# Kernel tuning notes

Measured on AMD Instinct MI355X. Metric: run time of the kernel, lower is better.

Reference implementation:

```python
import math
import jax, jax.numpy as jnp
import numpy as np

S, D_IN, H = 512, 256, 512  # seq_len(=num_events, window=1), input_dim, hidden_dim


def _ln(x, g, b, eps=1e-5):
    m = x.mean(-1, keepdims=True)
    v = ((x - m) ** 2).mean(-1, keepdims=True)
    return (x - m) * jax.lax.rsqrt(v + eps) * g + b


def setup_inputs() -> dict:
    key = jax.random.key(0)
    ks = jax.random.split(key, 16)
    p = lambda k, shp: (0.02 * jax.random.normal(k, shp, dtype=jnp.float32))
    return {
        "timestamps": jax.random.uniform(ks[0], (S,), dtype=jnp.float32),
        "features": jax.random.normal(ks[1], (S, D_IN), dtype=jnp.float32),
        "amplitudes": jax.random.uniform(ks[2], (S,), dtype=jnp.float32),
        "neuron_ids": jax.random.randint(ks[3], (S,), 0, 4096, dtype=jnp.int64 if jax.config.jax_enable_x64 else jnp.int32),
        # event_encoder: Linear(D_IN, H//2) -> ReLU -> Linear(H//2, H) -> LayerNorm(H)
        "We1": p(ks[4], (D_IN, H // 2)), "be1": jnp.zeros((H // 2,), jnp.float32),
        "We2": p(ks[5], (H // 2, H)), "be2": jnp.zeros((H,), jnp.float32),
        "g_ev": jnp.ones((H,), jnp.float32), "b_ev": jnp.zeros((H,), jnp.float32),
        # temporal_encoder: Linear(1, H//4) -> ReLU -> Linear(H//4, H//2)
        "Wt1": p(ks[6], (1, H // 4)), "bt1": jnp.zeros((H // 4,), jnp.float32),
        "Wt2": p(ks[7], (H // 4, H // 2)), "bt2": jnp.zeros((H // 2,), jnp.float32),
        # connectivity_proj: Linear(2H, H)  (used to map concat -> H)
        "Wc": p(ks[8], (2 * H, H)), "bc": jnp.zeros((H,), jnp.float32),
        # spike_rate_norm: LayerNorm(H)
        "g_sr": jnp.ones((H,), jnp.float32), "b_sr": jnp.zeros((H,), jnp.float32),
        # q/k/v projections Linear(H, H)
        "Wq": p(ks[9], (H, H)), "bq": jnp.zeros((H,), jnp.float32),
        "Wk": p(ks[10], (H, H)), "bk": jnp.zeros((H,), jnp.float32),
        "Wv": p(ks[11], (H, H)), "bv": jnp.zeros((H,), jnp.float32),
    }


def reference(timestamps, features, amplitudes, neuron_ids,
              We1, be1, We2, be2, g_ev, b_ev,
              Wt1, bt1, Wt2, bt2, Wc, bc, g_sr, b_sr,
              Wq, bq, Wk, bk, Wv, bv):
    s = features.shape[0]
    h_dim = Wq.shape[0]
    # _group_events_by_window with window_size=1: sort by timestamp
    order = jnp.argsort(timestamps)
    ts = timestamps[order]
    feats = features[order]
    amps = amplitudes[order]
    # event encoding: MLP + LayerNorm -> [S, H]
    h = jnp.maximum(feats @ We1 + be1, 0.0) @ We2 + be2
    h = _ln(h, g_ev, b_ev)
    # temporal encoding of raw timestamps -> [S, H/2], tiled to [S, H]
    t = jnp.maximum(ts[:, None] @ Wt1 + bt1, 0.0) @ Wt2 + bt2
    rep = h.shape[-1] // t.shape[-1]  # = 2
    comb = jnp.concatenate([h, jnp.tile(t, (1, rep))], axis=-1)  # [S, 2H]
    comb = comb * amps[:, None]                                   # amplitude gating
    comb = comb @ Wc + bc                                         # project 2H -> H
    comb = _ln(comb, g_sr, b_sr)
    # sinusoidal positional (temporal) encoding [S, H]
    pos = jnp.arange(s, dtype=jnp.float32)[:, None]
    div = jnp.exp(jnp.arange(0, h_dim, 2, dtype=jnp.float32) * (-math.log(10000.0) / h_dim))
    ang = pos * div  # [S, H/2]
    te = jnp.stack([jnp.sin(ang), jnp.cos(ang)], axis=-1).reshape(s, h_dim)
    ctx = (comb + te)[None]  # [1, S, H]
    # connectivity bias: 1 / (1 + |i - j|)  (vectorized; diagonal = 1 matches eye)
    idx = jnp.arange(s)
    conn = 1.0 / (1.0 + jnp.abs(idx[:, None] - idx[None, :]).astype(jnp.float32))  # [S, S]
    Q = ctx @ Wq + bq                                   # [1, S, H]
    K = ctx @ Wk + bk + conn[:, :, None] * 0.1          # broadcast -> [S, S, H]
    V = ctx @ Wv + bv                                   # [1, S, H]
    return Q, K, V
```

## Files before the change

### kernel.cpp

```cpp
#include <hip/hip_runtime.h>
#include <math.h>

#define S 512
#define DIN 256
#define H 512

typedef float f4 __attribute__((ext_vector_type(4)));

__global__ __launch_bounds__(512) void sort_kernel(
    const float* __restrict__ ts, const float* __restrict__ amp,
    int* __restrict__ order, float* __restrict__ ts_s, float* __restrict__ amp_s)
{
    __shared__ float sts[S];
    int i = threadIdx.x;
    sts[i] = ts[i];
    __syncthreads();
    float ti = sts[i];
    int rank = 0;
    for (int j = 0; j < S; ++j) {
        float tj = sts[j];
        rank += (tj < ti) || (tj == ti && j < i);
    }
    order[rank] = i;
    ts_s[rank]  = ti;
    amp_s[rank] = amp[i];
}

__device__ __forceinline__ void block_stats_512(float s, float ss, float* red,
                                                float& mean, float& inv)
{
    for (int off = 32; off > 0; off >>= 1) {
        s  += __shfl_down(s, off);
        ss += __shfl_down(ss, off);
    }
    int wid = threadIdx.x >> 6;
    if ((threadIdx.x & 63) == 0) { red[wid] = s; red[4 + wid] = ss; }
    __syncthreads();
    if (threadIdx.x == 0) {
        float Sm  = red[0] + red[1] + red[2] + red[3];
        float SSm = red[4] + red[5] + red[6] + red[7];
        float m = Sm * (1.0f / 512.0f);
        float v = SSm * (1.0f / 512.0f) - m * m;
        red[8] = m;
        red[9] = rsqrtf(v + 1e-5f);
    }
    __syncthreads();
    mean = red[8];
    inv  = red[9];
}

__global__ __launch_bounds__(256) void encoder_kernel(
    const int* __restrict__ order, const float* __restrict__ ts_s,
    const float* __restrict__ amp_s, const float* __restrict__ feats,
    const float* __restrict__ We1, const float* __restrict__ be1,
    const float* __restrict__ We2, const float* __restrict__ be2,
    const float* __restrict__ g_ev, const float* __restrict__ b_ev,
    const float* __restrict__ Wt1, const float* __restrict__ bt1,
    const float* __restrict__ Wt2, const float* __restrict__ bt2,
    const float* __restrict__ Wc, const float* __restrict__ bc,
    const float* __restrict__ g_sr, const float* __restrict__ b_sr,
    float* __restrict__ ctx)
{
    __shared__ float sf[DIN];
    __shared__ float sh1[256];
    __shared__ float sth[128];
    __shared__ float scomb[1024];
    __shared__ float red[16];

    int r = blockIdx.x;
    int t = threadIdx.x;
    int o = order[r];
    sf[t] = feats[o * DIN + t];
    float x = ts_s[r];
    if (t < 128) sth[t] = fmaxf(fmaf(x, Wt1[t], bt1[t]), 0.0f);
    __syncthreads();

    float acc = be1[t];
    #pragma unroll 4
    for (int d = 0; d < DIN; ++d) acc = fmaf(sf[d], We1[d * 256 + t], acc);
    sh1[t] = fmaxf(acc, 0.0f);
    __syncthreads();

    float a0 = be2[t], a1 = be2[t + 256];
    #pragma unroll 4
    for (int k = 0; k < 256; ++k) {
        float hv = sh1[k];
        a0 = fmaf(hv, We2[k * 512 + t], a0);
        a1 = fmaf(hv, We2[k * 512 + t + 256], a1);
    }
    float m, inv;
    block_stats_512(a0 + a1, a0 * a0 + a1 * a1, red, m, inv);
    float ampv = amp_s[r];
    scomb[t]       = fmaf((a0 - m) * inv, g_ev[t],       b_ev[t])       * ampv;
    scomb[t + 256] = fmaf((a1 - m) * inv, g_ev[t + 256], b_ev[t + 256]) * ampv;

    float tv = bt2[t];
    #pragma unroll 4
    for (int k = 0; k < 128; ++k) tv = fmaf(sth[k], Wt2[k * 256 + t], tv);
    tv *= ampv;
    scomb[512 + t] = tv;
    scomb[768 + t] = tv;
    __syncthreads();

    float c0 = bc[t], c1 = bc[t + 256];
    #pragma unroll 4
    for (int u = 0; u < 1024; ++u) {
        float uv = scomb[u];
        c0 = fmaf(uv, Wc[u * 512 + t], c0);
        c1 = fmaf(uv, Wc[u * 512 + t + 256], c1);
    }
    float m2, inv2;
    block_stats_512(c0 + c1, c0 * c0 + c1 * c1, red, m2, inv2);
    float e0 = fmaf((c0 - m2) * inv2, g_sr[t],       b_sr[t]);
    float e1 = fmaf((c1 - m2) * inv2, g_sr[t + 256], b_sr[t + 256]);

    const float NEG_LN1E4_OVER_H = -9.210340371976184f / 512.0f;
    float rf = (float)r;
    {
        int k0 = t >> 1;
        float ang0 = rf * expf((float)(2 * k0) * NEG_LN1E4_OVER_H);
        e0 += (t & 1) ? cosf(ang0) : sinf(ang0);
        int c = t + 256;
        int k1 = c >> 1;
        float ang1 = rf * expf((float)(2 * k1) * NEG_LN1E4_OVER_H);
        e1 += (c & 1) ? cosf(ang1) : sinf(ang1);
    }
    ctx[r * 512 + t]       = e0;
    ctx[r * 512 + t + 256] = e1;
}

__global__ __launch_bounds__(256) void qkv_kernel(
    const float* __restrict__ ctx,
    const float* __restrict__ Wq, const float* __restrict__ bq,
    const float* __restrict__ Wk, const float* __restrict__ bk,
    const float* __restrict__ Wv, const float* __restrict__ bv,
    float* __restrict__ Qout, float* __restrict__ Kbase, float* __restrict__ Vout)
{
    __shared__ float sc[4][512];
    int r0 = blockIdx.x * 4;
    int t = threadIdx.x;
    #pragma unroll
    for (int rr = 0; rr < 4; ++rr) {
        sc[rr][t]       = ctx[(r0 + rr) * 512 + t];
        sc[rr][t + 256] = ctx[(r0 + rr) * 512 + t + 256];
    }
    __syncthreads();

    float q0[4], q1[4], k0[4], k1[4], v0[4], v1[4];
    float bq0 = bq[t], bq1 = bq[t + 256];
    float bk0 = bk[t], bk1 = bk[t + 256];
    float bv0 = bv[t], bv1 = bv[t + 256];
    #pragma unroll
    for (int rr = 0; rr < 4; ++rr) {
        q0[rr] = bq0; q1[rr] = bq1;
        k0[rr] = bk0; k1[rr] = bk1;
        v0[rr] = bv0; v1[rr] = bv1;
    }
    #pragma unroll 2
    for (int h = 0; h < 512; ++h) {
        float wq0 = Wq[h * 512 + t], wq1 = Wq[h * 512 + t + 256];
        float wk0 = Wk[h * 512 + t], wk1 = Wk[h * 512 + t + 256];
        float wv0 = Wv[h * 512 + t], wv1 = Wv[h * 512 + t + 256];
        #pragma unroll
        for (int rr = 0; rr < 4; ++rr) {
            float cv = sc[rr][h];
            q0[rr] = fmaf(cv, wq0, q0[rr]);
            q1[rr] = fmaf(cv, wq1, q1[rr]);
            k0[rr] = fmaf(cv, wk0, k0[rr]);
            k1[rr] = fmaf(cv, wk1, k1[rr]);
            v0[rr] = fmaf(cv, wv0, v0[rr]);
            v1[rr] = fmaf(cv, wv1, v1[rr]);
        }
    }
    #pragma unroll
    for (int rr = 0; rr < 4; ++rr) {
        int r = r0 + rr;
        __builtin_nontemporal_store(q0[rr], &Qout[r * 512 + t]);
        __builtin_nontemporal_store(q1[rr], &Qout[r * 512 + t + 256]);
        Kbase[r * 512 + t]       = k0[rr];
        Kbase[r * 512 + t + 256] = k1[rr];
        __builtin_nontemporal_store(v0[rr], &Vout[r * 512 + t]);
        __builtin_nontemporal_store(v1[rr], &Vout[r * 512 + t + 256]);
    }
}

__global__ __launch_bounds__(128) void kexpand_kernel(
    const float* __restrict__ Kbase, float* __restrict__ Kout)
{
    __shared__ float sconn[1024];
    int j  = blockIdx.y;
    int i0 = blockIdx.x * 64;
    int t  = threadIdx.x;
    #pragma unroll
    for (int k = t; k < 1024; k += 128) sconn[k] = 0.1f / (float)(1 + k);
    f4 kb = ((const f4*)(Kbase + j * 512))[t];
    __syncthreads();
    f4* out = (f4*)Kout;
    size_t base = (size_t)j * 128 + t;
    #pragma unroll 8
    for (int ii = 0; ii < 64; ++ii) {
        int i = i0 + ii;
        int d = i - j; if (d < 0) d = -d;
        float conn = sconn[d];
        f4 v = kb + conn;
        out[base + (size_t)i * 65536] = v;
    }
}

extern "C" void kernel_launch(void* const* d_in, const int* in_sizes, int n_in,
                              void* d_out, int out_size, void* d_ws, size_t ws_size,
                              hipStream_t stream) {
    const float* timestamps = (const float*)d_in[0];
    const float* features   = (const float*)d_in[1];
    const float* amplitudes = (const float*)d_in[2];
    const float* We1 = (const float*)d_in[4];
    const float* be1 = (const float*)d_in[5];
    const float* We2 = (const float*)d_in[6];
    const float* be2 = (const float*)d_in[7];
    const float* g_ev = (const float*)d_in[8];
    const float* b_ev = (const float*)d_in[9];
    const float* Wt1 = (const float*)d_in[10];
    const float* bt1 = (const float*)d_in[11];
    const float* Wt2 = (const float*)d_in[12];
    const float* bt2 = (const float*)d_in[13];
    const float* Wc  = (const float*)d_in[14];
    const float* bc  = (const float*)d_in[15];
    const float* g_sr = (const float*)d_in[16];
    const float* b_sr = (const float*)d_in[17];
    const float* Wq = (const float*)d_in[18];
    const float* bq = (const float*)d_in[19];
    const float* Wk = (const float*)d_in[20];
    const float* bk = (const float*)d_in[21];
    const float* Wv = (const float*)d_in[22];
    const float* bv = (const float*)d_in[23];

    float* Qout = (float*)d_out;
    float* Kout = (float*)d_out + 262144;
    float* Vout = (float*)d_out + 262144 + 512 * 512 * 512;

    char* ws = (char*)d_ws;
    int*   order = (int*)ws;    ws += 512 * sizeof(int);
    float* ts_s  = (float*)ws;  ws += 512 * sizeof(float);
    float* amp_s = (float*)ws;  ws += 512 * sizeof(float);
    float* ctx   = (float*)ws;  ws += 262144 * sizeof(float);
    float* Kbase = (float*)ws;

    sort_kernel<<<1, 512, 0, stream>>>(timestamps, amplitudes, order, ts_s, amp_s);
    encoder_kernel<<<512, 256, 0, stream>>>(order, ts_s, amp_s, features,
        We1, be1, We2, be2, g_ev, b_ev, Wt1, bt1, Wt2, bt2, Wc, bc, g_sr, b_sr, ctx);
    qkv_kernel<<<128, 256, 0, stream>>>(ctx, Wq, bq, Wk, bk, Wv, bv, Qout, Kbase, Vout);
    kexpand_kernel<<<dim3(8, 512), 128, 0, stream>>>(Kbase, Kout);
}
```

Measured before the change: 912.4 us.

## Process two rows per encoder block and split QKV columns across blocks

The encoder kernel now handles two sequence rows per 512-thread block, so each weight load from We2 and Wc feeds two rows and halves weight traffic per row. The LayerNorm reduction computes statistics for both rows in one pass. The QKV kernel splits output columns over a second grid dimension, doubling block count to raise occupancy at the cost of reloading the ctx tile. Total time is likely dominated by the large K expansion write, which is unchanged.

```diff
diff --git a/kernel.cpp b/kernel.cpp
--- a/kernel.cpp
+++ b/kernel.cpp
@@ -26,30 +26,34 @@
     amp_s[rank] = amp[i];
 }
 
-__device__ __forceinline__ void block_stats_512(float s, float ss, float* red,
-                                                float& mean, float& inv)
-{
+__device__ __forceinline__ void block_stats2_512(float v0, float v1, float* red,
+    float& m0, float& i0, float& m1, float& i1)
+{
+    float s0 = v0, ss0 = v0 * v0, s1 = v1, ss1 = v1 * v1;
     for (int off = 32; off > 0; off >>= 1) {
-        s  += __shfl_down(s, off);
-        ss += __shfl_down(ss, off);
+        s0  += __shfl_down(s0, off);  ss0 += __shfl_down(ss0, off);
+        s1  += __shfl_down(s1, off);  ss1 += __shfl_down(ss1, off);
     }
     int wid = threadIdx.x >> 6;
-    if ((threadIdx.x & 63) == 0) { red[wid] = s; red[4 + wid] = ss; }
+    if ((threadIdx.x & 63) == 0) {
+        red[wid] = s0; red[8 + wid] = ss0; red[16 + wid] = s1; red[24 + wid] = ss1;
+    }
     __syncthreads();
     if (threadIdx.x == 0) {
-        float Sm  = red[0] + red[1] + red[2] + red[3];
-        float SSm = red[4] + red[5] + red[6] + red[7];
-        float m = Sm * (1.0f / 512.0f);
-        float v = SSm * (1.0f / 512.0f) - m * m;
-        red[8] = m;
-        red[9] = rsqrtf(v + 1e-5f);
-    }
-    __syncthreads();
-    mean = red[8];
-    inv  = red[9];
-}
-
-__global__ __launch_bounds__(256) void encoder_kernel(
+        float S0 = 0, SS0 = 0, S1 = 0, SS1 = 0;
+        #pragma unroll
+        for (int w = 0; w < 8; ++w) {
+            S0 += red[w]; SS0 += red[8 + w]; S1 += red[16 + w]; SS1 += red[24 + w];
+        }
+        float mm0 = S0 * (1.0f / 512.0f), mm1 = S1 * (1.0f / 512.0f);
+        red[32] = mm0; red[33] = rsqrtf(SS0 * (1.0f / 512.0f) - mm0 * mm0 + 1e-5f);
+        red[34] = mm1; red[35] = rsqrtf(SS1 * (1.0f / 512.0f) - mm1 * mm1 + 1e-5f);
+    }
+    __syncthreads();
+    m0 = red[32]; i0 = red[33]; m1 = red[34]; i1 = red[35];
+}
+
+__global__ __launch_bounds__(512) void encoder_kernel(
     const int* __restrict__ order, const float* __restrict__ ts_s,
     const float* __restrict__ amp_s, const float* __restrict__ feats,
     const float* __restrict__ We1, const float* __restrict__ be1,
@@ -61,72 +65,77 @@
     const float* __restrict__ g_sr, const float* __restrict__ b_sr,
     float* __restrict__ ctx)
 {
-    __shared__ float sf[DIN];
-    __shared__ float sh1[256];
-    __shared__ float sth[128];
-    __shared__ float scomb[1024];
-    __shared__ float red[16];
-
-    int r = blockIdx.x;
-    int t = threadIdx.x;
-    int o = order[r];
-    sf[t] = feats[o * DIN + t];
-    float x = ts_s[r];
-    if (t < 128) sth[t] = fmaxf(fmaf(x, Wt1[t], bt1[t]), 0.0f);
-    __syncthreads();
-
-    float acc = be1[t];
-    #pragma unroll 4
-    for (int d = 0; d < DIN; ++d) acc = fmaf(sf[d], We1[d * 256 + t], acc);
-    sh1[t] = fmaxf(acc, 0.0f);
-    __syncthreads();
-
-    float a0 = be2[t], a1 = be2[t + 256];
+    __shared__ float sf[2][DIN];
+    __shared__ float sh1[2][256];
+    __shared__ float sth[2][128];
+    __shared__ float scomb[2][1024];
+    __shared__ float red[36];
+
+    int r0 = blockIdx.x * 2;
+    int t  = threadIdx.x;
+    int o0 = order[r0], o1 = order[r0 + 1];
+    float x0 = ts_s[r0], x1 = ts_s[r0 + 1];
+    float amp0 = amp_s[r0], amp1 = amp_s[r0 + 1];
+
+    if (t < 256) sf[0][t] = feats[o0 * DIN + t];
+    else         sf[1][t - 256] = feats[o1 * DIN + (t - 256)];
+    if (t < 128)               sth[0][t]       = fmaxf(fmaf(x0, Wt1[t],       bt1[t]),       0.0f);
+    else if (t < 256)          sth[1][t - 128] = fmaxf(fmaf(x1, Wt1[t - 128], bt1[t - 128]), 0.0f);
+    __syncthreads();
+
+    {
+        int row = t >> 8, c = t & 255;
+        float acc = be1[c];
+        #pragma unroll 4
+        for (int d = 0; d < DIN; ++d) acc = fmaf(sf[row][d], We1[d * 256 + c], acc);
+        sh1[row][c] = fmaxf(acc, 0.0f);
+    }
+    __syncthreads();
+
+    float h0 = be2[t], h1 = be2[t];
     #pragma unroll 4
     for (int k = 0; k < 256; ++k) {
-        float hv = sh1[k];
-        a0 = fmaf(hv, We2[k * 512 + t], a0);
-        a1 = fmaf(hv, We2[k * 512 + t + 256], a1);
-    }
-    float m, inv;
-    block_stats_512(a0 + a1, a0 * a0 + a1 * a1, red, m, inv);
-    float ampv = amp_s[r];
-    scomb[t]       = fmaf((a0 - m) * inv, g_ev[t],       b_ev[t])       * ampv;
-    scomb[t + 256] = fmaf((a1 - m) * inv, g_ev[t + 256], b_ev[t + 256]) * ampv;
-
-    float tv = bt2[t];
-    #pragma unroll 4
-    for (int k = 0; k < 128; ++k) tv = fmaf(sth[k], Wt2[k * 256 + t], tv);
-    tv *= ampv;
-    scomb[512 + t] = tv;
-    scomb[768 + t] = tv;
-    __syncthreads();
-
-    float c0 = bc[t], c1 = bc[t + 256];
+        float w = We2[k * 512 + t];
+        h0 = fmaf(sh1[0][k], w, h0);
+        h1 = fmaf(sh1[1][k], w, h1);
+    }
+    float m0, inv0, m1, inv1;
+    block_stats2_512(h0, h1, red, m0, inv0, m1, inv1);
+    scomb[0][t] = fmaf((h0 - m0) * inv0, g_ev[t], b_ev[t]) * amp0;
+    scomb[1][t] = fmaf((h1 - m1) * inv1, g_ev[t], b_ev[t]) * amp1;
+
+    {
+        int row = t >> 8, c = t & 255;
+        float tv = bt2[c];
+        #pragma unroll 4
+        for (int k = 0; k < 128; ++k) tv = fmaf(sth[row][k], Wt2[k * 256 + c], tv);
+        tv *= (row ? amp1 : amp0);
+        scomb[row][512 + c] = tv;
+        scomb[row][768 + c] = tv;
+    }
+    __syncthreads();
+
+    float c0 = bc[t], c1 = bc[t];
     #pragma unroll 4
     for (int u = 0; u < 1024; ++u) {
-        float uv = scomb[u];
-        c0 = fmaf(uv, Wc[u * 512 + t], c0);
-        c1 = fmaf(uv, Wc[u * 512 + t + 256], c1);
-    }
-    float m2, inv2;
-    block_stats_512(c0 + c1, c0 * c0 + c1 * c1, red, m2, inv2);
-    float e0 = fmaf((c0 - m2) * inv2, g_sr[t],       b_sr[t]);
-    float e1 = fmaf((c1 - m2) * inv2, g_sr[t + 256], b_sr[t + 256]);
+        float w = Wc[u * 512 + t];
+        c0 = fmaf(scomb[0][u], w, c0);
+        c1 = fmaf(scomb[1][u], w, c1);
+    }
+    float n0, jnv0, n1, jnv1;
+    block_stats2_512(c0, c1, red, n0, jnv0, n1, jnv1);
+    float e0 = fmaf((c0 - n0) * jnv0, g_sr[t], b_sr[t]);
+    float e1 = fmaf((c1 - n1) * jnv1, g_sr[t], b_sr[t]);
 
     const float NEG_LN1E4_OVER_H = -9.210340371976184f / 512.0f;
-    float rf = (float)r;
     {
-        int k0 = t >> 1;
-        float ang0 = rf * expf((float)(2 * k0) * NEG_LN1E4_OVER_H);
-        e0 += (t & 1) ? cosf(ang0) : sinf(ang0);
-        int c = t + 256;
-        int k1 = c >> 1;
-        float ang1 = rf * expf((float)(2 * k1) * NEG_LN1E4_OVER_H);
-        e1 += (c & 1) ? cosf(ang1) : sinf(ang1);
-    }
-    ctx[r * 512 + t]       = e0;
-    ctx[r * 512 + t + 256] = e1;
+        float df = expf((float)(2 * (t >> 1)) * NEG_LN1E4_OVER_H);
+        float a0 = (float)r0 * df, a1 = (float)(r0 + 1) * df;
+        e0 += (t & 1) ? cosf(a0) : sinf(a0);
+        e1 += (t & 1) ? cosf(a1) : sinf(a1);
+    }
+    ctx[r0 * 512 + t]       = e0;
+    ctx[(r0 + 1) * 512 + t] = e1;
 }
 
 __global__ __launch_bounds__(256) void qkv_kernel(
@@ -137,8 +146,9 @@
     float* __restrict__ Qout, float* __restrict__ Kbase, float* __restrict__ Vout)
 {
     __shared__ float sc[4][512];
-    int r0 = blockIdx.x * 4;
-    int t = threadIdx.x;
+    int r0  = blockIdx.x * 4;
+    int t   = threadIdx.x;
+    int col = blockIdx.y * 256 + t;
     #pragma unroll
     for (int rr = 0; rr < 4; ++rr) {
         sc[rr][t]       = ctx[(r0 + rr) * 512 + t];
@@ -146,41 +156,30 @@
     }
     __syncthreads();
 
-    float q0[4], q1[4], k0[4], k1[4], v0[4], v1[4];
-    float bq0 = bq[t], bq1 = bq[t + 256];
-    float bk0 = bk[t], bk1 = bk[t + 256];
-    float bv0 = bv[t], bv1 = bv[t + 256];
-    #pragma unroll
-    for (int rr = 0; rr < 4; ++rr) {
-        q0[rr] = bq0; q1[rr] = bq1;
-        k0[rr] = bk0; k1[rr] = bk1;
-        v0[rr] = bv0; v1[rr] = bv1;
-    }
+    float q[4], k[4], v[4];
+    float bqc = bq[col], bkc = bk[col], bvc = bv[col];
+    #pragma unroll
+    for (int rr = 0; rr < 4; ++rr) { q[rr] = bqc; k[rr] = bkc; v[rr] = bvc; }
+
     #pragma unroll 2
     for (int h = 0; h < 512; ++h) {
-        float wq0 = Wq[h * 512 + t], wq1 = Wq[h * 512 + t + 256];
-        float wk0 = Wk[h * 512 + t], wk1 = Wk[h * 512 + t + 256];
-        float wv0 = Wv[h * 512 + t], wv1 = Wv[h * 512 + t + 256];
+        float wq = Wq[h * 512 + col];
+        float wk = Wk[h * 512 + col];
+        float wv = Wv[h * 512 + col];
         #pragma unroll
         for (int rr = 0; rr < 4; ++rr) {
             float cv = sc[rr][h];
-            q0[rr] = fmaf(cv, wq0, q0[rr]);
-            q1[rr] = fmaf(cv, wq1, q1[rr]);
-            k0[rr] = fmaf(cv, wk0, k0[rr]);
-            k1[rr] = fmaf(cv, wk1, k1[rr]);
-            v0[rr] = fmaf(cv, wv0, v0[rr]);
-            v1[rr] = fmaf(cv, wv1, v1[rr]);
+            q[rr] = fmaf(cv, wq, q[rr]);
+            k[rr] = fmaf(cv, wk, k[rr]);
+            v[rr] = fmaf(cv, wv, v[rr]);
         }
     }
     #pragma unroll
     for (int rr = 0; rr < 4; ++rr) {
         int r = r0 + rr;
-        __builtin_nontemporal_store(q0[rr], &Qout[r * 512 + t]);
-        __builtin_nontemporal_store(q1[rr], &Qout[r * 512 + t + 256]);
-        Kbase[r * 512 + t]       = k0[rr];
-        Kbase[r * 512 + t + 256] = k1[rr];
-        __builtin_nontemporal_store(v0[rr], &Vout[r * 512 + t]);
-        __builtin_nontemporal_store(v1[rr], &Vout[r * 512 + t + 256]);
+        __builtin_nontemporal_store(q[rr], &Qout[r * 512 + col]);
+        Kbase[r * 512 + col] = k[rr];
+        __builtin_nontemporal_store(v[rr], &Vout[r * 512 + col]);
     }
 }
 
@@ -246,8 +245,8 @@
     float* Kbase = (float*)ws;
 
     sort_kernel<<<1, 512, 0, stream>>>(timestamps, amplitudes, order, ts_s, amp_s);
-    encoder_kernel<<<512, 256, 0, stream>>>(order, ts_s, amp_s, features,
+    encoder_kernel<<<256, 512, 0, stream>>>(order, ts_s, amp_s, features,
         We1, be1, We2, be2, g_ev, b_ev, Wt1, bt1, Wt2, bt2, Wc, bc, g_sr, b_sr, ctx);
-    qkv_kernel<<<128, 256, 0, stream>>>(ctx, Wq, bq, Wk, bk, Wv, bv, Qout, Kbase, Vout);
+    qkv_kernel<<<dim3(128, 2), 256, 0, stream>>>(ctx, Wq, bq, Wk, bk, Wv, bv, Qout, Kbase, Vout);
     kexpand_kernel<<<dim3(8, 512), 128, 0, stream>>>(Kbase, Kout);
 }
```

Measured after the change: 897.9 us. Within noise of the previous version (-1.6%).
